# Kernel tuning notes

Measured on AMD Instinct MI355X. Metric: run time of the kernel, lower is better.

## Reference

```python
import math
import jax, jax.numpy as jnp
import numpy as np

WS = [2048, 4096, 8192]
RS = [1, 2, 4]
HEAD_IDX = 0


def build_indices(n):
    """Static dilated gather indices: concat of every segment's strided slice.

    Matches _prepare_sparse_indices for the chosen (ws, rs, n), which yields
    zero padding (each segment contributes exactly max_subatt_n indices).
    """
    max_m = min(n, max(w // r for w, r in zip(WS, RS)))
    parts = []
    for w, r in zip(WS, RS):
        offset = HEAD_IDX % r
        for s in range(0, n, w):
            seg = np.arange(s, min(s + w, n))[offset::r]
            assert len(seg) == max_m, "config chosen to avoid padding"
            parts.append(seg)
    return np.concatenate(parts).astype(np.int32), max_m


def _forward(x, Wq, Wk, Wv):
    b, n, c = x.shape
    idx_np, m = build_indices(n)
    idx = jnp.asarray(idx_np)            # [S], S = num_subatt * m
    S = idx_np.shape[0]
    nb = S // m                          # number of sub-attention windows

    # gather -> [b, S, c] -> batched windows [b*nb, m, c]
    bx = x[:, idx, :].reshape(b * nb, m, c)

    # single-head causal attention on each window, also return softmax denoms
    scale = 1.0 / math.sqrt(c)
    q = bx @ Wq
    k = bx @ Wk
    v = bx @ Wv
    logits = jnp.einsum('bqc,bkc->bqk', q, k) * scale
    causal = jnp.tril(jnp.ones((m, m), dtype=bool))
    logits = jnp.where(causal, logits, -jnp.inf)
    lse = jax.scipy.special.logsumexp(logits, axis=-1)   # [b*nb, m]
    probs = jnp.exp(logits - lse[..., None])
    o = jnp.einsum('bqk,bkc->bqc', probs, v)             # [b*nb, m, c]
    denoms = jnp.exp(lse)                                 # softmax denominators

    o = o.reshape(b, S, c)
    denoms = denoms.reshape(b, S)

    # _mix_outputs: scatter-add denoms per target position, reweight, scatter-add outputs
    denom_sums = jnp.zeros((b, n), x.dtype).at[:, idx].add(denoms)
    alphas = denoms / denom_sums[:, idx]                  # [b, S]
    out = jnp.zeros((b, n, c), x.dtype).at[:, idx, :].add(o * alphas[..., None])
    return out


def setup_inputs() -> dict:
    key = jax.random.key(0)
    kx, kq, kk, kv = jax.random.split(key, 4)
    b, n, c = 4, 8192, 64
    s = 1.0 / math.sqrt(c)
    return {
        'x': jax.random.normal(kx, (b, n, c), dtype=jnp.float32),
        'Wq': jax.random.normal(kq, (c, c), dtype=jnp.float32) * s,
        'Wk': jax.random.normal(kk, (c, c), dtype=jnp.float32) * s,
        'Wv': jax.random.normal(kv, (c, c), dtype=jnp.float32) * s,
    }


def reference(x, Wq, Wk, Wv):
    return _forward(x, Wq, Wk, Wv)
```

## Files before the change

### kernel.cpp

```cpp
#include <hip/hip_runtime.h>
#include <math.h>

#define NB   4
#define NSEQ 8192
#define CDIM 64
#define M    2048
#define NW   7
#define NBLK2 40

typedef _Float16 half8 __attribute__((ext_vector_type(8)));
typedef __fp16 fp16x2 __attribute__((ext_vector_type(2)));
typedef float f32x4 __attribute__((ext_vector_type(4)));
typedef unsigned short u16x4 __attribute__((ext_vector_type(4)));

#if defined(__has_builtin) && __has_builtin(__builtin_amdgcn_exp2f)
#define EXP2(x) __builtin_amdgcn_exp2f(x)
#else
#define EXP2(x) __expf((x) * 0.69314718056f)
#endif

#define QSCALE 0.1803368801111204f
#define PBIAS 4.0f

#define K_OFF   0
#define VT_OFF  8192
#define VT_STRIDE 80
#define VT_BUF  5120
#define PS0_OFF 18432
#define PS1_OFF 23552
#define PS_STRIDE 80

__device__ __forceinline__ int win_base(int w) {
    return (w < 4) ? (w << 11) : ((w < 6) ? ((w - 4) << 12) : 0);
}
__device__ __forceinline__ int win_stride(int w) {
    return (w < 4) ? 1 : ((w < 6) ? 2 : 4);
}

__global__ __launch_bounds__(256, 1) void qkv_proj(
        const float* __restrict__ x,
        const float* __restrict__ Wq, const float* __restrict__ Wk,
        const float* __restrict__ Wv,
        _Float16* __restrict__ Qg, _Float16* __restrict__ Kg,
        _Float16* __restrict__ Vg) {
    const int t = threadIdx.x;
    const int wid = t >> 6, lane = t & 63, l15 = lane & 15, quad = lane >> 4;

    half8 wb[3][2][4];
#pragma unroll
    for (int m = 0; m < 3; ++m) {
        const float* Wm = (m == 0) ? Wq : ((m == 1) ? Wk : Wv);
        const float sc = (m == 0) ? QSCALE : 1.0f;
#pragma unroll
        for (int kh = 0; kh < 2; ++kh)
#pragma unroll
            for (int nt = 0; nt < 4; ++nt) {
                float f[8];
#pragma unroll
                for (int j = 0; j < 8; ++j)
                    f[j] = Wm[(kh * 32 + quad * 8 + j) * 64 + nt * 16 + l15] * sc;
                union { fp16x2 h[4]; half8 v; } u;
#pragma unroll
                for (int p = 0; p < 4; ++p)
                    u.h[p] = __builtin_amdgcn_cvt_pkrtz(f[2 * p], f[2 * p + 1]);
                wb[m][kh][nt] = u.v;
            }
    }

    const int rowbase = blockIdx.x * 128 + wid * 32;
#pragma unroll
    for (int mt = 0; mt < 2; ++mt) {
        const int r0 = rowbase + mt * 16;
        half8 xa[2];
#pragma unroll
        for (int kh = 0; kh < 2; ++kh) {
            const float* xr = x + (size_t)(r0 + l15) * 64 + kh * 32 + quad * 8;
            const float4 a = *(const float4*)xr;
            const float4 b2 = *(const float4*)(xr + 4);
            union { fp16x2 h[4]; half8 v; } u;
            u.h[0] = __builtin_amdgcn_cvt_pkrtz(a.x, a.y);
            u.h[1] = __builtin_amdgcn_cvt_pkrtz(a.z, a.w);
            u.h[2] = __builtin_amdgcn_cvt_pkrtz(b2.x, b2.y);
            u.h[3] = __builtin_amdgcn_cvt_pkrtz(b2.z, b2.w);
            xa[kh] = u.v;
        }
#pragma unroll
        for (int m = 0; m < 3; ++m) {
            f32x4 acc[4];
#pragma unroll
            for (int nt = 0; nt < 4; ++nt) {
                acc[nt] = (f32x4){0.f, 0.f, 0.f, 0.f};
                acc[nt] = __builtin_amdgcn_mfma_f32_16x16x32_f16(xa[0], wb[m][0][nt], acc[nt], 0, 0, 0);
                acc[nt] = __builtin_amdgcn_mfma_f32_16x16x32_f16(xa[1], wb[m][1][nt], acc[nt], 0, 0, 0);
            }
            _Float16* outp = (m == 0) ? Qg : ((m == 1) ? Kg : Vg);
#pragma unroll
            for (int nt = 0; nt < 4; ++nt)
#pragma unroll
                for (int j = 0; j < 4; ++j)
                    outp[(size_t)(r0 + quad * 4 + j) * 64 + nt * 16 + l15] =
                        (_Float16)acc[nt][j];
        }
    }
}

__global__ __launch_bounds__(256, 4) void attn(
        const _Float16* __restrict__ Qg, const _Float16* __restrict__ Kg,
        const _Float16* __restrict__ Vg,
        _Float16* __restrict__ Op, float* __restrict__ LSEp) {
    __shared__ __align__(16) char smem[28672];

    int id = 39 - (int)blockIdx.x;
    int QT, ci;
    if (id < 4)       { QT = id;              ci = 0; }
    else if (id < 12) { int r = id - 4;  QT = 4  + (r >> 1); ci = r & 1; }
    else if (id < 24) { int r = id - 12; int q3 = r / 3; QT = 8 + q3; ci = r - 3 * q3; }
    else              { int r = id - 24; QT = 12 + (r >> 2); ci = r & 3; }
    const int w = blockIdx.y, b = blockIdx.z;
    const int base = win_base(w), stride = win_stride(w);
    const int g = QT >> 2;
    const int cb = 2 * g * (g + 1) + (QT & 3) * (g + 1);
    const int outblk = (b * NW + w) * NBLK2 + cb + ci;
    const int kt0 = ci * 16;
    const int ktmax = 4 * QT + 4;
    const int kt1 = (kt0 + 16 < ktmax) ? kt0 + 16 : ktmax;

    const _Float16* Qb = Qg + (size_t)b * NSEQ * 64;
    const _Float16* Kb = Kg + (size_t)b * NSEQ * 64;
    const _Float16* Vb = Vg + (size_t)b * NSEQ * 64;

    const int t = threadIdx.x;
    const int wid = t >> 6, lane = t & 63, l15 = lane & 15, quad = lane >> 4;

    const int sr = t >> 3, sch = t & 7;
    const int c4 = t & 15, kq = t >> 4;
    const int vd0 = 4 * c4;

    const size_t qr0 = (size_t)(base + stride * (QT * 128 + 16 * wid + l15)) * 64;
    const size_t qr1 = (size_t)(base + stride * (QT * 128 + 64 + 16 * wid + l15)) * 64;
    const half8 qa00 = *(const half8*)(Qb + qr0 + quad * 8);
    const half8 qa01 = *(const half8*)(Qb + qr0 + 32 + quad * 8);
    const half8 qa10 = *(const half8*)(Qb + qr1 + quad * 8);
    const half8 qa11 = *(const half8*)(Qb + qr1 + 32 + quad * 8);

    f32x4 oacc0[4], oacc1[4];
    float l_[8];
#pragma unroll
    for (int ns = 0; ns < 4; ++ns) {
        oacc0[ns] = (f32x4){0.f, 0.f, 0.f, 0.f};
        oacc1[ns] = (f32x4){0.f, 0.f, 0.f, 0.f};
    }
#pragma unroll
    for (int j = 0; j < 8; ++j) l_[j] = 0.f;

    half8 pk;
    u16x4 pv0, pv1;

    {
        const size_t ka = (size_t)(base + stride * (kt0 * 32 + sr)) * 64 + sch * 8;
        pk = *(const half8*)(Kb + ka);
        const size_t va = (size_t)(base + stride * (kt0 * 32 + kq)) * 64 + vd0;
        pv0 = *(const u16x4*)(Vb + va);
        pv1 = *(const u16x4*)(Vb + va + (size_t)stride * 16 * 64);
        char* Kd = smem + K_OFF;
        char* Vd = smem + VT_OFF;
        *(half8*)(Kd + sr * 128 + ((sch ^ (sr & 7)) * 16)) = pk;
#pragma unroll
        for (int i = 0; i < 4; ++i) {
            int d = vd0 + i;
            unsigned int pkw = (unsigned int)pv0[i] | ((unsigned int)pv1[i] << 16);
            int ch = ((kq >> 2) ^ (d >> 4) ^ (d & 3) ^ ((d >> 2) & 3)) & 3;
            *(unsigned int*)(Vd + d * VT_STRIDE + ch * 16 + (kq & 3) * 4) = pkw;
        }
    }

    int cur = 0;
    for (int kt = kt0; kt < kt1; ++kt) {
        __syncthreads();
        const bool pf = (kt + 1 < kt1);
        if (pf) {
            const size_t ka = (size_t)(base + stride * ((kt + 1) * 32 + sr)) * 64 + sch * 8;
            pk = *(const half8*)(Kb + ka);
            const size_t va = (size_t)(base + stride * ((kt + 1) * 32 + kq)) * 64 + vd0;
            pv0 = *(const u16x4*)(Vb + va);
            pv1 = *(const u16x4*)(Vb + va + (size_t)stride * 16 * 64);
        }

        const char* Kd = smem + K_OFF + cur * 4096;
        const char* Vd = smem + VT_OFF + cur * VT_BUF;
        char* Ps0 = smem + PS0_OFF;
        char* Ps1 = smem + PS1_OFF;

        half8 kb[2][2];
#pragma unroll
        for (int ns = 0; ns < 2; ++ns) {
            const int krow = ns * 16 + l15, swk = krow & 7;
            kb[ns][0] = *(const half8*)(Kd + krow * 128 + ((quad ^ swk) * 16));
            kb[ns][1] = *(const half8*)(Kd + krow * 128 + (((quad + 4) ^ swk) * 16));
        }
        f32x4 sa0[2], sa1[2];
        __builtin_amdgcn_s_setprio(1);
#pragma unroll
        for (int ns = 0; ns < 2; ++ns) {
            f32x4 c0 = (f32x4){0.f, 0.f, 0.f, 0.f};
            c0 = __builtin_amdgcn_mfma_f32_16x16x32_f16(qa00, kb[ns][0], c0, 0, 0, 0);
            c0 = __builtin_amdgcn_mfma_f32_16x16x32_f16(qa01, kb[ns][1], c0, 0, 0, 0);
            sa0[ns] = c0;
            f32x4 c1 = (f32x4){0.f, 0.f, 0.f, 0.f};
            c1 = __builtin_amdgcn_mfma_f32_16x16x32_f16(qa10, kb[ns][0], c1, 0, 0, 0);
            c1 = __builtin_amdgcn_mfma_f32_16x16x32_f16(qa11, kb[ns][1], c1, 0, 0, 0);
            sa1[ns] = c1;
        }
        __builtin_amdgcn_s_setprio(0);
        if (kt >= 4 * QT) {
            const int colb = kt * 32 + l15;
            const int row0 = QT * 128 + 16 * wid + quad * 4;
#pragma unroll
            for (int ns = 0; ns < 2; ++ns)
#pragma unroll
                for (int j = 0; j < 4; ++j) {
                    if (colb + ns * 16 > row0 + j)      sa0[ns][j] = -1e30f;
                    if (colb + ns * 16 > row0 + 64 + j) sa1[ns][j] = -1e30f;
                }
        }

        half8 vb[4];
#pragma unroll
        for (int ns = 0; ns < 4; ++ns) {
            const int d = ns * 16 + l15;
            const int ch = (quad ^ (d >> 4) ^ (d & 3) ^ ((d >> 2) & 3)) & 3;
            vb[ns] = *(const half8*)(Vd + d * VT_STRIDE + ch * 16);
        }

#pragma unroll
        for (int j = 0; j < 4; ++j) {
            const int q = 16 * wid + quad * 4 + j;
            float p0 = EXP2(sa0[0][j] - PBIAS);
            float p1 = EXP2(sa0[1][j] - PBIAS);
            l_[j] += p0 + p1;
            union { fp16x2 h; unsigned int u; } pw;
            pw.h = __builtin_amdgcn_cvt_pkrtz(p0, p1);
            const int ch = ((l15 >> 2) ^ (q & 3) ^ ((q >> 2) & 3)) & 3;
            *(unsigned int*)(Ps0 + q * PS_STRIDE + ch * 16 + (l15 & 3) * 4) = pw.u;
        }
#pragma unroll
        for (int j = 0; j < 4; ++j) {
            const int q = 16 * wid + quad * 4 + j;
            float p0 = EXP2(sa1[0][j] - PBIAS);
            float p1 = EXP2(sa1[1][j] - PBIAS);
            l_[4 + j] += p0 + p1;
            union { fp16x2 h; unsigned int u; } pw;
            pw.h = __builtin_amdgcn_cvt_pkrtz(p0, p1);
            const int ch = ((l15 >> 2) ^ (q & 3) ^ ((q >> 2) & 3)) & 3;
            *(unsigned int*)(Ps1 + q * PS_STRIDE + ch * 16 + (l15 & 3) * 4) = pw.u;
        }
        {
            const int qp = 16 * wid + l15;
            const int ch = (quad ^ (qp & 3) ^ ((qp >> 2) & 3)) & 3;
            half8 pa0 = *(const half8*)(Ps0 + qp * PS_STRIDE + ch * 16);
            half8 pa1 = *(const half8*)(Ps1 + qp * PS_STRIDE + ch * 16);
            __builtin_amdgcn_s_setprio(1);
#pragma unroll
            for (int ns = 0; ns < 4; ++ns)
                oacc0[ns] = __builtin_amdgcn_mfma_f32_16x16x32_f16(pa0, vb[ns], oacc0[ns], 0, 0, 0);
#pragma unroll
            for (int ns = 0; ns < 4; ++ns)
                oacc1[ns] = __builtin_amdgcn_mfma_f32_16x16x32_f16(pa1, vb[ns], oacc1[ns], 0, 0, 0);
            __builtin_amdgcn_s_setprio(0);
        }

        if (pf) {
            char* Kn = smem + K_OFF + (cur ^ 1) * 4096;
            char* Vn = smem + VT_OFF + (cur ^ 1) * VT_BUF;
            *(half8*)(Kn + sr * 128 + ((sch ^ (sr & 7)) * 16)) = pk;
#pragma unroll
            for (int i = 0; i < 4; ++i) {
                int d = vd0 + i;
                unsigned int pkw = (unsigned int)pv0[i] | ((unsigned int)pv1[i] << 16);
                int ch = ((kq >> 2) ^ (d >> 4) ^ (d & 3) ^ ((d >> 2) & 3)) & 3;
                *(unsigned int*)(Vn + d * VT_STRIDE + ch * 16 + (kq & 3) * 4) = pkw;
            }
        }
        cur ^= 1;
    }

#pragma unroll
    for (int j = 0; j < 8; ++j) {
        float s = l_[j];
        s += __shfl_xor(s, 1, 16);
        s += __shfl_xor(s, 2, 16);
        s += __shfl_xor(s, 4, 16);
        s += __shfl_xor(s, 8, 16);
        l_[j] = s;
    }
    const int qrow0 = 16 * wid + quad * 4;
    if (l15 == 0) {
#pragma unroll
        for (int j = 0; j < 4; ++j) {
            LSEp[(size_t)outblk * 128 + qrow0 + j]      = __logf(l_[j]);
            LSEp[(size_t)outblk * 128 + 64 + qrow0 + j] = __logf(l_[4 + j]);
        }
    }
#pragma unroll
    for (int j = 0; j < 4; ++j) {
        const float inv0 = 1.0f / l_[j];
        const float inv1 = 1.0f / l_[4 + j];
        const size_t r0off = ((size_t)outblk * 128 + qrow0 + j) * 64 + l15;
        const size_t r1off = ((size_t)outblk * 128 + 64 + qrow0 + j) * 64 + l15;
#pragma unroll
        for (int ns = 0; ns < 4; ++ns) {
            Op[r0off + ns * 16] = (_Float16)(oacc0[ns][j] * inv0);
            Op[r1off + ns * 16] = (_Float16)(oacc1[ns][j] * inv1);
        }
    }
}

typedef _Float16 half8v __attribute__((ext_vector_type(8)));
__global__ __launch_bounds__(256) void mix_out(
        const _Float16* __restrict__ Op, const float* __restrict__ LSEp,
        float* __restrict__ out) {
    int gid = blockIdx.x * 256 + threadIdx.x;
    int f8 = gid & 7;
    int tpos = (gid >> 3) & (NSEQ - 1);
    int b = gid >> 16;

    int idx[12];
    float lse[12];

    {
        int w = tpos >> 11, j = tpos & (M - 1);
        int QT = j >> 7, gg = QT >> 2, q = j & 127;
        int cbase = 2 * gg * (gg + 1) + (QT & 3) * (gg + 1);
        int bb = ((b * NW + w) * NBLK2 + cbase) * 128 + q;
        int cmax = j >> 9;
#pragma unroll
        for (int c = 0; c < 4; ++c) {
            int cc = (c <= cmax) ? c : cmax;
            idx[c] = bb + cc * 128;
            float v = LSEp[idx[c]];
            lse[c] = (c <= cmax) ? v : -1e30f;
        }
    }
    {
        int act = ((tpos & 1) == 0);
        int w = 4 + (tpos >> 12), j = (tpos & 4095) >> 1;
        int QT = j >> 7, gg = QT >> 2, q = j & 127;
        int cbase = 2 * gg * (gg + 1) + (QT & 3) * (gg + 1);
        int bb = ((b * NW + w) * NBLK2 + cbase) * 128 + q;
        int cmax = j >> 9;
#pragma unroll
        for (int c = 0; c < 4; ++c) {
            int cc = (c <= cmax) ? c : cmax;
            idx[4 + c] = bb + cc * 128;
            float v = LSEp[idx[4 + c]];
            lse[4 + c] = (act && c <= cmax) ? v : -1e30f;
        }
    }
    {
        int act = ((tpos & 3) == 0);
        int j = tpos >> 2;
        int QT = j >> 7, gg = QT >> 2, q = j & 127;
        int cbase = 2 * gg * (gg + 1) + (QT & 3) * (gg + 1);
        int bb = ((b * NW + 6) * NBLK2 + cbase) * 128 + q;
        int cmax = j >> 9;
#pragma unroll
        for (int c = 0; c < 4; ++c) {
            int cc = (c <= cmax) ? c : cmax;
            idx[8 + c] = bb + cc * 128;
            float v = LSEp[idx[8 + c]];
            lse[8 + c] = (act && c <= cmax) ? v : -1e30f;
        }
    }

    half8v v[12];
#pragma unroll
    for (int i = 0; i < 12; ++i)
        v[i] = *(const half8v*)(Op + (size_t)idx[i] * 64 + f8 * 8);

    float Mx = -1e30f;
#pragma unroll
    for (int i = 0; i < 12; ++i) Mx = fmaxf(Mx, lse[i]);

    float acc[8];
#pragma unroll
    for (int k = 0; k < 8; ++k) acc[k] = 0.f;
    float wsum = 0.f;
#pragma unroll
    for (int i = 0; i < 12; ++i) {
        float a = __expf(lse[i] - Mx);
        wsum += a;
#pragma unroll
        for (int k = 0; k < 8; ++k) acc[k] += a * (float)v[i][k];
    }
    float inv = 1.0f / wsum;
    size_t o = ((size_t)b * NSEQ + tpos) * 64 + f8 * 8;
    float4 r0 = make_float4(acc[0] * inv, acc[1] * inv, acc[2] * inv, acc[3] * inv);
    float4 r1 = make_float4(acc[4] * inv, acc[5] * inv, acc[6] * inv, acc[7] * inv);
    *(float4*)&out[o] = r0;
    *(float4*)&out[o + 4] = r1;
}

extern "C" void kernel_launch(void* const* d_in, const int* in_sizes, int n_in,
                              void* d_out, int out_size, void* d_ws, size_t ws_size,
                              hipStream_t stream) {
    const float* x  = (const float*)d_in[0];
    const float* Wq = (const float*)d_in[1];
    const float* Wk = (const float*)d_in[2];
    const float* Wv = (const float*)d_in[3];
    float* out = (float*)d_out;

    const size_t QN = (size_t)NB * NSEQ * CDIM;
    _Float16* Qg = (_Float16*)d_ws;
    _Float16* Kg = Qg + QN;
    _Float16* Vg = Kg + QN;
    _Float16* Op = Vg + QN;
    float* LSEp  = (float*)(Op + (size_t)NB * NW * NBLK2 * 128 * 64);

    qkv_proj<<<NB * NSEQ / 128, 256, 0, stream>>>(x, Wq, Wk, Wv, Qg, Kg, Vg);
    attn<<<dim3(NBLK2, NW, NB), 256, 0, stream>>>(Qg, Kg, Vg, Op, LSEp);
    mix_out<<<(NB * NSEQ * 8) / 256, 256, 0, stream>>>(Op, LSEp, out);
}
```

Measured before the change: 121.5 us.

## Compute transposed QK^T so probabilities feed PV MFMA directly from registers

Swaps the MFMA operand order in the score computation so each lane holds scores in the layout the P·V MFMA A-operand expects. The exp'd probabilities are then packed straight into a half8 register operand, removing the LDS write/read round trip through the P staging buffers and shrinking shared memory. Row sums now reduce across quads instead of within 16 lanes, and are redistributed with shuffles for the final normalisation. The causal mask indexing is rewritten to match the transposed layout.

```diff
diff --git a/kernel.cpp b/kernel.cpp
--- a/kernel.cpp
+++ b/kernel.cpp
@@ -26,9 +26,6 @@
 #define VT_OFF  8192
 #define VT_STRIDE 80
 #define VT_BUF  5120
-#define PS0_OFF 18432
-#define PS1_OFF 23552
-#define PS_STRIDE 80
 
 __device__ __forceinline__ int win_base(int w) {
     return (w < 4) ? (w << 11) : ((w < 6) ? ((w - 4) << 12) : 0);
@@ -108,7 +105,7 @@
         const _Float16* __restrict__ Qg, const _Float16* __restrict__ Kg,
         const _Float16* __restrict__ Vg,
         _Float16* __restrict__ Op, float* __restrict__ LSEp) {
-    __shared__ __align__(16) char smem[28672];
+    __shared__ __align__(16) char smem[18432];
 
     int id = 39 - (int)blockIdx.x;
     int QT, ci;
@@ -144,14 +141,12 @@
     const half8 qa11 = *(const half8*)(Qb + qr1 + 32 + quad * 8);
 
     f32x4 oacc0[4], oacc1[4];
-    float l_[8];
+    float l0 = 0.f, l1 = 0.f;
 #pragma unroll
     for (int ns = 0; ns < 4; ++ns) {
         oacc0[ns] = (f32x4){0.f, 0.f, 0.f, 0.f};
         oacc1[ns] = (f32x4){0.f, 0.f, 0.f, 0.f};
     }
-#pragma unroll
-    for (int j = 0; j < 8; ++j) l_[j] = 0.f;
 
     half8 pk;
     u16x4 pv0, pv1;
@@ -188,8 +183,6 @@
 
         const char* Kd = smem + K_OFF + cur * 4096;
         const char* Vd = smem + VT_OFF + cur * VT_BUF;
-        char* Ps0 = smem + PS0_OFF;
-        char* Ps1 = smem + PS1_OFF;
 
         half8 kb[2][2];
 #pragma unroll
@@ -203,24 +196,24 @@
 #pragma unroll
         for (int ns = 0; ns < 2; ++ns) {
             f32x4 c0 = (f32x4){0.f, 0.f, 0.f, 0.f};
-            c0 = __builtin_amdgcn_mfma_f32_16x16x32_f16(qa00, kb[ns][0], c0, 0, 0, 0);
-            c0 = __builtin_amdgcn_mfma_f32_16x16x32_f16(qa01, kb[ns][1], c0, 0, 0, 0);
+            c0 = __builtin_amdgcn_mfma_f32_16x16x32_f16(kb[ns][0], qa00, c0, 0, 0, 0);
+            c0 = __builtin_amdgcn_mfma_f32_16x16x32_f16(kb[ns][1], qa01, c0, 0, 0, 0);
             sa0[ns] = c0;
             f32x4 c1 = (f32x4){0.f, 0.f, 0.f, 0.f};
-            c1 = __builtin_amdgcn_mfma_f32_16x16x32_f16(qa10, kb[ns][0], c1, 0, 0, 0);
-            c1 = __builtin_amdgcn_mfma_f32_16x16x32_f16(qa11, kb[ns][1], c1, 0, 0, 0);
+            c1 = __builtin_amdgcn_mfma_f32_16x16x32_f16(kb[ns][0], qa10, c1, 0, 0, 0);
+            c1 = __builtin_amdgcn_mfma_f32_16x16x32_f16(kb[ns][1], qa11, c1, 0, 0, 0);
             sa1[ns] = c1;
         }
         __builtin_amdgcn_s_setprio(0);
         if (kt >= 4 * QT) {
-            const int colb = kt * 32 + l15;
-            const int row0 = QT * 128 + 16 * wid + quad * 4;
+            const int q0 = QT * 128 + 16 * wid + l15 - kt * 32;
+            const int kvb = quad * 4;
 #pragma unroll
             for (int ns = 0; ns < 2; ++ns)
 #pragma unroll
                 for (int j = 0; j < 4; ++j) {
-                    if (colb + ns * 16 > row0 + j)      sa0[ns][j] = -1e30f;
-                    if (colb + ns * 16 > row0 + 64 + j) sa1[ns][j] = -1e30f;
+                    if (kvb + ns * 16 + j > q0)      sa0[ns][j] = -1e30f;
+                    if (kvb + ns * 16 + j > q0 + 64) sa1[ns][j] = -1e30f;
                 }
         }
 
@@ -232,40 +225,34 @@
             vb[ns] = *(const half8*)(Vd + d * VT_STRIDE + ch * 16);
         }
 
-#pragma unroll
-        for (int j = 0; j < 4; ++j) {
-            const int q = 16 * wid + quad * 4 + j;
-            float p0 = EXP2(sa0[0][j] - PBIAS);
-            float p1 = EXP2(sa0[1][j] - PBIAS);
-            l_[j] += p0 + p1;
-            union { fp16x2 h; unsigned int u; } pw;
-            pw.h = __builtin_amdgcn_cvt_pkrtz(p0, p1);
-            const int ch = ((l15 >> 2) ^ (q & 3) ^ ((q >> 2) & 3)) & 3;
-            *(unsigned int*)(Ps0 + q * PS_STRIDE + ch * 16 + (l15 & 3) * 4) = pw.u;
-        }
-#pragma unroll
-        for (int j = 0; j < 4; ++j) {
-            const int q = 16 * wid + quad * 4 + j;
-            float p0 = EXP2(sa1[0][j] - PBIAS);
-            float p1 = EXP2(sa1[1][j] - PBIAS);
-            l_[4 + j] += p0 + p1;
-            union { fp16x2 h; unsigned int u; } pw;
-            pw.h = __builtin_amdgcn_cvt_pkrtz(p0, p1);
-            const int ch = ((l15 >> 2) ^ (q & 3) ^ ((q >> 2) & 3)) & 3;
-            *(unsigned int*)(Ps1 + q * PS_STRIDE + ch * 16 + (l15 & 3) * 4) = pw.u;
-        }
         {
-            const int qp = 16 * wid + l15;
-            const int ch = (quad ^ (qp & 3) ^ ((qp >> 2) & 3)) & 3;
-            half8 pa0 = *(const half8*)(Ps0 + qp * PS_STRIDE + ch * 16);
-            half8 pa1 = *(const half8*)(Ps1 + qp * PS_STRIDE + ch * 16);
+            union { fp16x2 h[4]; half8 v; } pu;
+#pragma unroll
+            for (int u = 0; u < 4; ++u) {
+                float pA = EXP2(sa0[0][u] - PBIAS);
+                float pB = EXP2(sa0[1][u] - PBIAS);
+                l0 += pA + pB;
+                pu.h[u] = __builtin_amdgcn_cvt_pkrtz(pA, pB);
+            }
             __builtin_amdgcn_s_setprio(1);
 #pragma unroll
             for (int ns = 0; ns < 4; ++ns)
-                oacc0[ns] = __builtin_amdgcn_mfma_f32_16x16x32_f16(pa0, vb[ns], oacc0[ns], 0, 0, 0);
+                oacc0[ns] = __builtin_amdgcn_mfma_f32_16x16x32_f16(pu.v, vb[ns], oacc0[ns], 0, 0, 0);
+            __builtin_amdgcn_s_setprio(0);
+        }
+        {
+            union { fp16x2 h[4]; half8 v; } pu;
+#pragma unroll
+            for (int u = 0; u < 4; ++u) {
+                float pA = EXP2(sa1[0][u] - PBIAS);
+                float pB = EXP2(sa1[1][u] - PBIAS);
+                l1 += pA + pB;
+                pu.h[u] = __builtin_amdgcn_cvt_pkrtz(pA, pB);
+            }
+            __builtin_amdgcn_s_setprio(1);
 #pragma unroll
             for (int ns = 0; ns < 4; ++ns)
-                oacc1[ns] = __builtin_amdgcn_mfma_f32_16x16x32_f16(pa1, vb[ns], oacc1[ns], 0, 0, 0);
+                oacc1[ns] = __builtin_amdgcn_mfma_f32_16x16x32_f16(pu.v, vb[ns], oacc1[ns], 0, 0, 0);
             __builtin_amdgcn_s_setprio(0);
         }
 
@@ -284,27 +271,19 @@
         cur ^= 1;
     }
 
-#pragma unroll
-    for (int j = 0; j < 8; ++j) {
-        float s = l_[j];
-        s += __shfl_xor(s, 1, 16);
-        s += __shfl_xor(s, 2, 16);
-        s += __shfl_xor(s, 4, 16);
-        s += __shfl_xor(s, 8, 16);
-        l_[j] = s;
+    l0 += __shfl_xor(l0, 16, 64);
+    l0 += __shfl_xor(l0, 32, 64);
+    l1 += __shfl_xor(l1, 16, 64);
+    l1 += __shfl_xor(l1, 32, 64);
+    if (quad == 0) {
+        LSEp[(size_t)outblk * 128 + 16 * wid + l15]      = __logf(l0);
+        LSEp[(size_t)outblk * 128 + 64 + 16 * wid + l15] = __logf(l1);
     }
     const int qrow0 = 16 * wid + quad * 4;
-    if (l15 == 0) {
-#pragma unroll
-        for (int j = 0; j < 4; ++j) {
-            LSEp[(size_t)outblk * 128 + qrow0 + j]      = __logf(l_[j]);
-            LSEp[(size_t)outblk * 128 + 64 + qrow0 + j] = __logf(l_[4 + j]);
-        }
-    }
 #pragma unroll
     for (int j = 0; j < 4; ++j) {
-        const float inv0 = 1.0f / l_[j];
-        const float inv1 = 1.0f / l_[4 + j];
+        const float inv0 = 1.0f / __shfl(l0, quad * 4 + j, 64);
+        const float inv1 = 1.0f / __shfl(l1, quad * 4 + j, 64);
         const size_t r0off = ((size_t)outblk * 128 + qrow0 + j) * 64 + l15;
         const size_t r1off = ((size_t)outblk * 128 + 64 + qrow0 + j) * 64 + l15;
 #pragma unroll
```

After: 113.2 us. -6.8%, faster.
